# Kernel tuning notes

Hardware: AMD Instinct MI355X
Metric: run time of the kernel (lower is better)

## Reference

```python
import jax, jax.numpy as jnp
import numpy as np

B, H, E = 64, 768, 128


def setup_inputs() -> dict:
    key = jax.random.key(0)
    k0, k1, k2, k3, k4, k5 = jax.random.split(key, 6)
    s = 1.0 / np.sqrt(H).astype(np.float32)
    return {
        "head_src": jax.random.normal(k0, (B, H), dtype=jnp.float32),
        "rel_src": jax.random.normal(k1, (B, H), dtype=jnp.float32),
        "tail_src": jax.random.normal(k2, (B, H), dtype=jnp.float32),
        "W_e": jax.random.normal(k3, (E, H), dtype=jnp.float32) * s,
        "b_e": jnp.zeros((E,), dtype=jnp.float32),
        "W_r": jax.random.normal(k4, (E, H), dtype=jnp.float32) * s,
        "b_r": jnp.zeros((E,), dtype=jnp.float32),
        # core tensor init mirrors np.random.uniform(-1, 1, (E, E, E))
        "core": jax.random.uniform(k5, (E, E, E), dtype=jnp.float32, minval=-1.0, maxval=1.0),
    }


def reference(head_src, rel_src, tail_src, W_e, b_e, W_r, b_r, core):
    # forward(): entity / relation projections (nn.Linear)
    head = head_src @ W_e.T + b_e          # [B, E]
    tail = tail_src @ W_e.T + b_e          # [B, E]
    rel = rel_src @ W_r.T + b_r            # [B, E]

    # energy(): faithful replication of the broadcast multiply+sum sequence.
    # head/rel/tail all broadcast along core dim 0 due to the unsqueeze pattern.
    w = (core[None] * head[:, :, None, None]).sum(-1)   # [B, E, E] (via [B,E,E,E] intermediate)
    w = (w * rel[:, :, None]).sum(-1)                   # [B, E]
    energy = -(w * tail).sum(-1)                        # [B]
    return energy
```

## Files before the change

kernel.cpp:

```cpp
#include <hip/hip_runtime.h>

#define HDIM 768
#define EDIM 128
#define BDIM 64

#define NCORE_BLOCKS 1024
#define NPROJ_BLOCKS 768

__global__ __launch_bounds__(256) void fused_kernel(
    const float* __restrict__ core,
    const float* __restrict__ head_src, const float* __restrict__ rel_src,
    const float* __restrict__ tail_src,
    const float* __restrict__ W_e, const float* __restrict__ b_e,
    const float* __restrict__ W_r, const float* __restrict__ b_r,
    float* __restrict__ partials, float* __restrict__ P) {
    __shared__ float wpart[4];
    const int blk = blockIdx.x;
    const int t = threadIdx.x;
    const int wave = t >> 6, lane = t & 63;

    if (blk < NCORE_BLOCKS) {
        const int i     = blk >> 3;
        const int chunk = blk & 7;
        const float4* p = (const float4*)(core + (size_t)i * 16384 + (size_t)chunk * 2048);
        float4 a = p[t];
        float4 b = p[t + 256];
        float s = (a.x + a.y) + (a.z + a.w) + (b.x + b.y) + (b.z + b.w);
        for (int off = 32; off; off >>= 1) s += __shfl_down(s, off, 64);
        if (lane == 0) wpart[wave] = s;
        __syncthreads();
        if (t == 0) partials[blk] = (wpart[0] + wpart[1]) + (wpart[2] + wpart[3]);
    } else {
        const int pid = blk - NCORE_BLOCKS;
        const int wg  = pid * 4 + wave;
        const int ich = wg & 15;
        const int mb  = wg >> 4;
        const int m   = mb >> 6;
        const int b   = mb & 63;

        const float* src  = (m == 0) ? head_src : (m == 1) ? rel_src : tail_src;
        const float* W    = (m == 1) ? W_r : W_e;
        const float* bias = (m == 1) ? b_r : b_e;

        const float4* s4 = (const float4*)(src + b * HDIM);
        const float4 x0 = s4[lane], x1 = s4[lane + 64], x2 = s4[lane + 128];

        const int i0 = ich * 8;
#pragma unroll
        for (int u = 0; u < 8; ++u) {
            const int i = i0 + u;
            const float4* w4 = (const float4*)(W + i * HDIM);
            const float4 w0 = w4[lane], w1 = w4[lane + 64], w2 = w4[lane + 128];
            float d = w0.x * x0.x + w0.y * x0.y + w0.z * x0.z + w0.w * x0.w
                    + w1.x * x1.x + w1.y * x1.y + w1.z * x1.z + w1.w * x1.w
                    + w2.x * x2.x + w2.y * x2.y + w2.z * x2.z + w2.w * x2.w;
            for (int off = 32; off; off >>= 1) d += __shfl_down(d, off, 64);
            if (lane == 0) P[(m * BDIM + b) * EDIM + i] = d + bias[i];
        }
    }
}

__global__ __launch_bounds__(128) void final_kernel(
    const float* __restrict__ partials, const float* __restrict__ P,
    float* __restrict__ out) {
    const int b = blockIdx.x;
    const int i = threadIdx.x;

    float S = 0.f;
#pragma unroll
    for (int c = 0; c < 8; ++c) S += partials[i * 8 + c];

    const float h = P[(0 * BDIM + b) * EDIM + i];
    const float r = P[(1 * BDIM + b) * EDIM + i];
    const float tt = P[(2 * BDIM + b) * EDIM + i];
    float val = S * h * r * tt;

    for (int off = 32; off; off >>= 1) val += __shfl_down(val, off, 64);
    __shared__ float wsum[2];
    if ((i & 63) == 0) wsum[i >> 6] = val;
    __syncthreads();
    if (i == 0) out[b] = -(wsum[0] + wsum[1]);
}

extern "C" void kernel_launch(void* const* d_in, const int* in_sizes, int n_in,
                              void* d_out, int out_size, void* d_ws, size_t ws_size,
                              hipStream_t stream) {
    const float* head_src = (const float*)d_in[0];
    const float* rel_src  = (const float*)d_in[1];
    const float* tail_src = (const float*)d_in[2];
    const float* W_e      = (const float*)d_in[3];
    const float* b_e      = (const float*)d_in[4];
    const float* W_r      = (const float*)d_in[5];
    const float* b_r      = (const float*)d_in[6];
    const float* core     = (const float*)d_in[7];
    float* out      = (float*)d_out;
    float* partials = (float*)d_ws;
    float* P        = (float*)d_ws + NCORE_BLOCKS;

    fused_kernel<<<NCORE_BLOCKS + NPROJ_BLOCKS, 256, 0, stream>>>(
        core, head_src, rel_src, tail_src, W_e, b_e, W_r, b_r, partials, P);
    final_kernel<<<BDIM, 128, 0, stream>>>(partials, P, out);
}
```

Baseline: 80.10 us.

## Fuse final reduction into main kernel via last-block atomic counter

Merges the final energy reduction into the main kernel. Each block bumps a global atomic counter, and the last block to finish computes all outputs, which removes the second kernel launch. The core row-sum blocks also shrink from 1024 to 256, with each block summing four chunks, so fewer blocks are launched. The cost is that one block does the whole final reduction serially, and correctness now depends on release/acquire fences and on resetting the counter at the end of each call.

```diff
diff --git a/kernel.cpp b/kernel.cpp
--- a/kernel.cpp
+++ b/kernel.cpp
@@ -4,100 +4,137 @@
 #define EDIM 128
 #define BDIM 64
 
-#define NCORE_BLOCKS 1024
+#define NCORE_BLOCKS 256
 #define NPROJ_BLOCKS 768
+#define NBLOCKS (NCORE_BLOCKS + NPROJ_BLOCKS)
 
-__global__ __launch_bounds__(256) void fused_kernel(
+__device__ unsigned int g_count = 0;
+
+__global__ __launch_bounds__(256) void fused_all(
     const float* __restrict__ core,
     const float* __restrict__ head_src, const float* __restrict__ rel_src,
     const float* __restrict__ tail_src,
     const float* __restrict__ W_e, const float* __restrict__ b_e,
     const float* __restrict__ W_r, const float* __restrict__ b_r,
-    float* __restrict__ partials, float* __restrict__ P) {
-    __shared__ float wpart[4];
-    const int blk = blockIdx.x;
-    const int t = threadIdx.x;
-    const int wave = t >> 6, lane = t & 63;
+    float* __restrict__ partials, float* __restrict__ P,
+    float* __restrict__ out) {
+  __shared__ float wpart[4][4];
+  __shared__ float s_S[EDIM];
+  __shared__ int s_last;
+  const int blk = blockIdx.x;
+  const int t = threadIdx.x;
+  const int wave = t >> 6, lane = t & 63;
 
-    if (blk < NCORE_BLOCKS) {
-        const int i     = blk >> 3;
-        const int chunk = blk & 7;
-        const float4* p = (const float4*)(core + (size_t)i * 16384 + (size_t)chunk * 2048);
-        float4 a = p[t];
-        float4 b = p[t + 256];
-        float s = (a.x + a.y) + (a.z + a.w) + (b.x + b.y) + (b.z + b.w);
-        for (int off = 32; off; off >>= 1) s += __shfl_down(s, off, 64);
-        if (lane == 0) wpart[wave] = s;
-        __syncthreads();
-        if (t == 0) partials[blk] = (wpart[0] + wpart[1]) + (wpart[2] + wpart[3]);
-    } else {
-        const int pid = blk - NCORE_BLOCKS;
-        const int wg  = pid * 4 + wave;
-        const int ich = wg & 15;
-        const int mb  = wg >> 4;
-        const int m   = mb >> 6;
-        const int b   = mb & 63;
+  if (blk < NCORE_BLOCKS) {
+    const int i = blk >> 1;
+    const int half = blk & 1;
+    const float* base = core + (size_t)i * (EDIM * EDIM) + (size_t)half * 8192;
+    float s[4];
+#pragma unroll
+    for (int u = 0; u < 4; ++u) {
+      const float4* p = (const float4*)(base + u * 2048);
+      const float4 a = p[t];
+      const float4 b = p[t + 256];
+      s[u] = (a.x + a.y) + (a.z + a.w) + (b.x + b.y) + (b.z + b.w);
+    }
+#pragma unroll
+    for (int off = 32; off; off >>= 1) {
+#pragma unroll
+      for (int u = 0; u < 4; ++u) s[u] += __shfl_down(s[u], off, 64);
+    }
+    if (lane == 0) {
+#pragma unroll
+      for (int u = 0; u < 4; ++u) wpart[u][wave] = s[u];
+    }
+    __syncthreads();
+    if (t < 4)
+      partials[i * 8 + half * 4 + t] =
+          (wpart[t][0] + wpart[t][1]) + (wpart[t][2] + wpart[t][3]);
+  } else {
+    const int pid = blk - NCORE_BLOCKS;
+    const int wg = pid * 4 + wave;
+    const int ich = wg & 15;
+    const int mb = wg >> 4;
+    const int m = mb >> 6;
+    const int b = mb & 63;
 
-        const float* src  = (m == 0) ? head_src : (m == 1) ? rel_src : tail_src;
-        const float* W    = (m == 1) ? W_r : W_e;
-        const float* bias = (m == 1) ? b_r : b_e;
+    const float* src  = (m == 0) ? head_src : (m == 1) ? rel_src : tail_src;
+    const float* W    = (m == 1) ? W_r : W_e;
+    const float* bias = (m == 1) ? b_r : b_e;
 
-        const float4* s4 = (const float4*)(src + b * HDIM);
-        const float4 x0 = s4[lane], x1 = s4[lane + 64], x2 = s4[lane + 128];
+    const float4* s4 = (const float4*)(src + b * HDIM);
+    const float4 x0 = s4[lane], x1 = s4[lane + 64], x2 = s4[lane + 128];
 
-        const int i0 = ich * 8;
+    const int i0 = ich * 8;
 #pragma unroll
-        for (int u = 0; u < 8; ++u) {
-            const int i = i0 + u;
-            const float4* w4 = (const float4*)(W + i * HDIM);
-            const float4 w0 = w4[lane], w1 = w4[lane + 64], w2 = w4[lane + 128];
-            float d = w0.x * x0.x + w0.y * x0.y + w0.z * x0.z + w0.w * x0.w
-                    + w1.x * x1.x + w1.y * x1.y + w1.z * x1.z + w1.w * x1.w
-                    + w2.x * x2.x + w2.y * x2.y + w2.z * x2.z + w2.w * x2.w;
-            for (int off = 32; off; off >>= 1) d += __shfl_down(d, off, 64);
-            if (lane == 0) P[(m * BDIM + b) * EDIM + i] = d + bias[i];
-        }
+    for (int u = 0; u < 8; ++u) {
+      const int i = i0 + u;
+      const float4* w4 = (const float4*)(W + i * HDIM);
+      const float4 w0 = w4[lane], w1 = w4[lane + 64], w2 = w4[lane + 128];
+      float d = w0.x * x0.x + w0.y * x0.y + w0.z * x0.z + w0.w * x0.w
+              + w1.x * x1.x + w1.y * x1.y + w1.z * x1.z + w1.w * x1.w
+              + w2.x * x2.x + w2.y * x2.y + w2.z * x2.z + w2.w * x2.w;
+#pragma unroll
+      for (int off = 32; off; off >>= 1) d += __shfl_down(d, off, 64);
+      if (lane == 0) P[(m * BDIM + b) * EDIM + i] = d + bias[i];
     }
-}
+  }
 
-__global__ __launch_bounds__(128) void final_kernel(
-    const float* __restrict__ partials, const float* __restrict__ P,
-    float* __restrict__ out) {
-    const int b = blockIdx.x;
-    const int i = threadIdx.x;
+  __builtin_amdgcn_fence(__ATOMIC_RELEASE, "agent");
+  __syncthreads();
+  if (t == 0) {
+    const unsigned int old = atomicAdd(&g_count, 1u);
+    s_last = (old == (unsigned int)(NBLOCKS - 1));
+  }
+  __syncthreads();
+  if (!s_last) return;
+  __builtin_amdgcn_fence(__ATOMIC_ACQUIRE, "agent");
 
+  if (t < EDIM) {
     float S = 0.f;
 #pragma unroll
-    for (int c = 0; c < 8; ++c) S += partials[i * 8 + c];
+    for (int c = 0; c < 8; ++c) S += partials[t * 8 + c];
+    s_S[t] = S;
+  }
+  __syncthreads();
 
-    const float h = P[(0 * BDIM + b) * EDIM + i];
-    const float r = P[(1 * BDIM + b) * EDIM + i];
-    const float tt = P[(2 * BDIM + b) * EDIM + i];
-    float val = S * h * r * tt;
+#pragma unroll 2
+  for (int bb = 0; bb < 16; ++bb) {
+    const int b = wave * 16 + bb;
+    const float hL = P[(0 * BDIM + b) * EDIM + lane];
+    const float rL = P[(1 * BDIM + b) * EDIM + lane];
+    const float tL = P[(2 * BDIM + b) * EDIM + lane];
+    const float hH = P[(0 * BDIM + b) * EDIM + lane + 64];
+    const float rH = P[(1 * BDIM + b) * EDIM + lane + 64];
+    const float tH = P[(2 * BDIM + b) * EDIM + lane + 64];
+    float vL = s_S[lane] * hL * rL * tL;
+    float vH = s_S[lane + 64] * hH * rH * tH;
+#pragma unroll
+    for (int off = 32; off; off >>= 1) {
+      vL += __shfl_down(vL, off, 64);
+      vH += __shfl_down(vH, off, 64);
+    }
+    if (lane == 0) out[b] = -(vL + vH);
+  }
 
-    for (int off = 32; off; off >>= 1) val += __shfl_down(val, off, 64);
-    __shared__ float wsum[2];
-    if ((i & 63) == 0) wsum[i >> 6] = val;
-    __syncthreads();
-    if (i == 0) out[b] = -(wsum[0] + wsum[1]);
+  if (t == 0) g_count = 0;
 }
 
 extern "C" void kernel_launch(void* const* d_in, const int* in_sizes, int n_in,
                               void* d_out, int out_size, void* d_ws, size_t ws_size,
                               hipStream_t stream) {
-    const float* head_src = (const float*)d_in[0];
-    const float* rel_src  = (const float*)d_in[1];
-    const float* tail_src = (const float*)d_in[2];
-    const float* W_e      = (const float*)d_in[3];
-    const float* b_e      = (const float*)d_in[4];
-    const float* W_r      = (const float*)d_in[5];
-    const float* b_r      = (const float*)d_in[6];
-    const float* core     = (const float*)d_in[7];
-    float* out      = (float*)d_out;
-    float* partials = (float*)d_ws;
-    float* P        = (float*)d_ws + NCORE_BLOCKS;
+  const float* head_src = (const float*)d_in[0];
+  const float* rel_src  = (const float*)d_in[1];
+  const float* tail_src = (const float*)d_in[2];
+  const float* W_e      = (const float*)d_in[3];
+  const float* b_e      = (const float*)d_in[4];
+  const float* W_r      = (const float*)d_in[5];
+  const float* b_r      = (const float*)d_in[6];
+  const float* core     = (const float*)d_in[7];
+  float* out      = (float*)d_out;
+  float* partials = (float*)d_ws;
+  float* P        = (float*)d_ws + 1024;
 
-    fused_kernel<<<NCORE_BLOCKS + NPROJ_BLOCKS, 256, 0, stream>>>(
-        core, head_src, rel_src, tail_src, W_e, b_e, W_r, b_r, partials, P);
-    final_kernel<<<BDIM, 128, 0, stream>>>(partials, P, out);
+  fused_all<<<NBLOCKS, 256, 0, stream>>>(
+      core, head_src, rel_src, tail_src, W_e, b_e, W_r, b_r, partials, P, out);
 }
```

Measured after the change: 126.2 us. 1.57x slower.
